# Kernel tuning notes

Hardware: AMD Instinct MI355X
Metric: run time of the kernel (lower is better)

Reference implementation:

```python
import jax, jax.numpy as jnp
import numpy as np

GAMMA = 20
LAMBDA_INV = 25.0


def setup_inputs() -> dict:
    key = jax.random.key(0)
    k1, k2 = jax.random.split(key)
    B, P, D = 128, 512, 384
    z = jax.random.normal(k1, (B, P, D), dtype=jnp.float32)
    view_ids = jax.random.randint(k2, (P,), 0, 2, dtype=jnp.int64)
    return {"z": z, "view_ids": view_ids}


def reference(z, view_ids):
    B, P, D = z.shape
    # [B, P, P] pairwise similarity per image
    sim = jnp.einsum('bpd,bqd->bpq', z, z)
    # valid pairs: different view and not self
    mask_view = view_ids[None, :] != view_ids[:, None]          # [P, P]
    mask = mask_view & ~jnp.eye(P, dtype=bool)
    sim = jnp.where(mask[None, :, :], sim, jnp.float32(-1.0))
    best_sim = sim.max(axis=2)                                   # [B, P]
    best_j = sim.argmax(axis=2)                                  # [B, P]
    # flatten across batch, global top-gamma anchors
    best_sim_flat = best_sim.reshape(-1)                         # [B*P]
    offsets = jnp.arange(B, dtype=best_j.dtype)[:, None] * P
    best_j_flat = (best_j + offsets).reshape(-1)                 # [B*P]
    topk_vals, topk_idx = jax.lax.top_k(best_sim_flat, GAMMA)
    z_flat = z.reshape(-1, D)
    z1 = z_flat[topk_idx]                                        # anchors
    z2 = z_flat[best_j_flat[topk_idx]]                           # matches
    loss = LAMBDA_INV * jnp.mean((z1 - z2) ** 2)
    fmatch_avg_cos = jax.lax.stop_gradient(topk_vals.mean())
    return loss, fmatch_avg_cos
```

## Files before the change

kernel.cpp:

```cpp
#include <hip/hip_runtime.h>


#define NB 128
#define NP 512
#define ND 384
#define NGAMMA 20
#define NKS 12

typedef __attribute__((ext_vector_type(8))) short short8;
typedef __attribute__((ext_vector_type(4))) float f32x4;

__device__ __forceinline__ unsigned short f2bf(float f) {
    unsigned int u = __float_as_uint(f);
    u += 0x7fffu + ((u >> 16) & 1u);
    return (unsigned short)(u >> 16);
}

__device__ __forceinline__ void gload16(const void* gptr, void* lptr) {
    __builtin_amdgcn_global_load_lds(
        (const __attribute__((address_space(1))) void*)gptr,
        (__attribute__((address_space(3))) void*)lptr, 16, 0, 0);
}

__global__ __launch_bounds__(256) void fm_convert(
    const float* __restrict__ z, unsigned short* __restrict__ zhi)
{
    size_t i = (size_t)blockIdx.x * 256 + threadIdx.x;
    const float4* zp = (const float4*)z + i * 2;
    float4 v0 = zp[0], v1 = zp[1];
    float f[8] = {v0.x, v0.y, v0.z, v0.w, v1.x, v1.y, v1.z, v1.w};
    short8 s;
#pragma unroll
    for (int j = 0; j < 8; ++j) s[j] = (short)f2bf(f[j]);
    *(short8*)&zhi[i * 8] = s;
}

__global__ __launch_bounds__(256, 3) void fm_gemm(
    const unsigned short* __restrict__ zhi, const int* __restrict__ view,
    float* __restrict__ pval, int* __restrict__ pidx)
{
    __shared__ __align__(16) unsigned short Ah[3][4][128][8];
    __shared__ __align__(16) unsigned short Bh[3][4][128][8];
    __shared__ int vs[NP];
    float* lsv = (float*)&Ah[0][0][0][0];
    int*   lsi = (int*)lsv + 256;
    float* lqv = (float*)((int*)lsv + 512);
    int*   lqi = (int*)lsv + 768;

    const int tid  = threadIdx.x;
    const int lane = tid & 63;
    const int wid  = tid >> 6;
    const int wr   = wid >> 1, wc = wid & 1;
    const int g    = lane >> 4, r = lane & 15;

    const int bid  = blockIdx.x;
    const int gidx = (bid & 7) * 160 + (bid >> 3);
    const int b    = gidx / 10;
    const int t    = gidx % 10;
    int tr, tc;
    if (t < 4)      { tr = 0; tc = t; }
    else if (t < 7) { tr = 1; tc = t - 3; }
    else if (t < 9) { tr = 2; tc = t - 5; }
    else            { tr = 3; tc = 3; }
    const bool diag = (tr == tc);
    const int p0 = tr * 128, q0 = tc * 128;

    vs[tid]       = view[tid];
    vs[tid + 256] = view[tid + 256];
    __builtin_amdgcn_sched_barrier(0);

    const size_t zb = (size_t)b * NP * ND;

    f32x4 acc[4][4];
#pragma unroll
    for (int mi = 0; mi < 4; ++mi)
#pragma unroll
        for (int ni = 0; ni < 4; ++ni) acc[mi][ni] = (f32x4){0.f, 0.f, 0.f, 0.f};

#define STAGE(BUF, KT)                                                           \
    do {                                                                         \
        _Pragma("unroll")                                                        \
        for (int i = 0; i < 2; ++i) {                                            \
            const int c_  = wid * 2 + i;                                         \
            const int kg_ = c_ >> 1;                                             \
            const int rb_ = (c_ & 1) * 64;                                       \
            gload16(zhi + zb + (size_t)(p0 + rb_ + lane) * ND + (KT) * 32 + kg_ * 8, \
                    &Ah[BUF][kg_][rb_][0]);                                      \
            gload16(zhi + zb + (size_t)(q0 + rb_ + lane) * ND + (KT) * 32 + kg_ * 8, \
                    &Bh[BUF][kg_][rb_][0]);                                      \
        }                                                                        \
    } while (0)

#define COMPUTE(BUF)                                                             \
    do {                                                                         \
        short8 ah_[4], bh_[4];                                                   \
        _Pragma("unroll")                                                        \
        for (int mi = 0; mi < 4; ++mi)                                           \
            ah_[mi] = *(const short8*)&Ah[BUF][g][wr * 64 + mi * 16 + r][0];     \
        _Pragma("unroll")                                                        \
        for (int ni = 0; ni < 4; ++ni)                                           \
            bh_[ni] = *(const short8*)&Bh[BUF][g][wc * 64 + ni * 16 + r][0];     \
        _Pragma("unroll")                                                        \
        for (int mi = 0; mi < 4; ++mi)                                           \
            _Pragma("unroll")                                                    \
            for (int ni = 0; ni < 4; ++ni)                                       \
                acc[mi][ni] = __builtin_amdgcn_mfma_f32_16x16x32_bf16(           \
                    ah_[mi], bh_[ni], acc[mi][ni], 0, 0, 0);                     \
    } while (0)

    STAGE(0, 0);
    STAGE(1, 1);
#pragma unroll
    for (int kt = 0; kt < NKS; ++kt) {
        if (kt < NKS - 1) asm volatile("s_waitcnt vmcnt(4)" ::: "memory");
        else              asm volatile("s_waitcnt vmcnt(0)" ::: "memory");
        __builtin_amdgcn_s_barrier();
        __builtin_amdgcn_sched_barrier(0);
        if (kt + 2 < NKS) STAGE((kt + 2) % 3, kt + 2);
        __builtin_amdgcn_sched_barrier(0);
        COMPUTE(kt % 3);
    }
#undef STAGE
#undef COMPUTE

#pragma unroll
    for (int mi = 0; mi < 4; ++mi) {
#pragma unroll
        for (int j = 0; j < 4; ++j) {
            const int prow = p0 + wr * 64 + mi * 16 + g * 4 + j;
            const int rv = vs[prow];
            float bv = -2.0f; int bq = 0;
#pragma unroll
            for (int ni = 0; ni < 4; ++ni) {
                const int q = q0 + wc * 64 + ni * 16 + r;
                const float v = (vs[q] != rv) ? acc[mi][ni][j] : -1.0f;
                if (v > bv) { bv = v; bq = q; }
            }
#pragma unroll
            for (int off = 1; off < 16; off <<= 1) {
                const float ov = __shfl_xor(bv, off);
                const int   oq = __shfl_xor(bq, off);
                if (ov > bv || (ov == bv && oq < bq)) { bv = ov; bq = oq; }
            }
            if (r == 0) {
                lsv[(wr * 2 + wc) * 64 + mi * 16 + g * 4 + j] = bv;
                lsi[(wr * 2 + wc) * 64 + mi * 16 + g * 4 + j] = bq;
            }
        }
    }
    if (!diag) {
#pragma unroll
        for (int ni = 0; ni < 4; ++ni) {
            const int q = q0 + wc * 64 + ni * 16 + r;
            const int qv = vs[q];
            float bv = -2.0f; int bp = 0;
#pragma unroll
            for (int mi = 0; mi < 4; ++mi)
#pragma unroll
                for (int j = 0; j < 4; ++j) {
                    const int prow = p0 + wr * 64 + mi * 16 + g * 4 + j;
                    const float v = (vs[prow] != qv) ? acc[mi][ni][j] : -1.0f;
                    if (v > bv) { bv = v; bp = prow; }
                }
#pragma unroll
            for (int off = 16; off < 64; off <<= 1) {
                const float ov = __shfl_xor(bv, off);
                const int   op = __shfl_xor(bp, off);
                if (ov > bv || (ov == bv && op < bp)) { bv = ov; bp = op; }
            }
            if (g == 0) {
                lqv[(wc * 2 + wr) * 64 + ni * 16 + r] = bv;
                lqi[(wc * 2 + wr) * 64 + ni * 16 + r] = bp;
            }
        }
    }
    __syncthreads();
    if (tid < 128) {
        const int half = tid >> 6, row = tid & 63;
        {
            float v0 = lsv[(half * 2 + 0) * 64 + row]; int i0 = lsi[(half * 2 + 0) * 64 + row];
            const float v1 = lsv[(half * 2 + 1) * 64 + row]; const int i1 = lsi[(half * 2 + 1) * 64 + row];
            if (v1 > v0) { v0 = v1; i0 = i1; }
            const int p = p0 + half * 64 + row;
            pval[((size_t)b * NP + p) * 4 + tc] = v0;
            pidx[((size_t)b * NP + p) * 4 + tc] = i0;
        }
        if (!diag) {
            float v0 = lqv[(half * 2 + 0) * 64 + row]; int i0 = lqi[(half * 2 + 0) * 64 + row];
            const float v1 = lqv[(half * 2 + 1) * 64 + row]; const int i1 = lqi[(half * 2 + 1) * 64 + row];
            if (v1 > v0) { v0 = v1; i0 = i1; }
            const int q = q0 + half * 64 + row;
            pval[((size_t)b * NP + q) * 4 + tr] = v0;
            pidx[((size_t)b * NP + q) * 4 + tr] = i0;
        }
    }
}

__global__ __launch_bounds__(64) void fm_topk_local(
    const float* __restrict__ pval, float* __restrict__ cval, int* __restrict__ cidx)
{
    const int lane = threadIdx.x;
    const int base = blockIdx.x * 1024;
    float v[16]; int id[16];
#pragma unroll
    for (int i = 0; i < 16; ++i) {
        const int a = base + i * 64 + lane;
        const float4 pv = ((const float4*)pval)[a];
        float bv = pv.x;
        if (pv.y > bv) bv = pv.y;
        if (pv.z > bv) bv = pv.z;
        if (pv.w > bv) bv = pv.w;
        v[i] = bv; id[i] = a;
    }
    for (int it = 0; it < NGAMMA; ++it) {
        float bv = v[0]; int bi = id[0];
#pragma unroll
        for (int i = 1; i < 16; ++i)
            if (v[i] > bv || (v[i] == bv && id[i] < bi)) { bv = v[i]; bi = id[i]; }
#pragma unroll
        for (int off = 1; off < 64; off <<= 1) {
            const float ov = __shfl_xor(bv, off);
            const int   oi = __shfl_xor(bi, off);
            if (ov > bv || (ov == bv && oi < bi)) { bv = ov; bi = oi; }
        }
        if (lane == 0) {
            cval[blockIdx.x * NGAMMA + it] = bv;
            cidx[blockIdx.x * NGAMMA + it] = bi;
        }
#pragma unroll
        for (int i = 0; i < 16; ++i) if (id[i] == bi) v[i] = -1e30f;
    }
}

__global__ __launch_bounds__(256) void fm_final(
    const float* __restrict__ cval, const int* __restrict__ cidx,
    const float* __restrict__ pval, const int* __restrict__ pidx,
    const float* __restrict__ z, float* __restrict__ out)
{
    __shared__ int sel[NGAMMA];
    __shared__ int selj[NGAMMA];
    __shared__ float red[4];

    const int t = threadIdx.x;
    const int lane = t & 63, w = t >> 6;
    float ssum = 0.f;

    if (w == 0) {
        float v[20]; int id[20];
#pragma unroll
        for (int i = 0; i < 20; ++i) {
            const int e = i * 64 + lane;
            v[i] = cval[e]; id[i] = cidx[e];
        }
        for (int it = 0; it < NGAMMA; ++it) {
            float bv = v[0]; int bi = id[0];
#pragma unroll
            for (int i = 1; i < 20; ++i)
                if (v[i] > bv || (v[i] == bv && id[i] < bi)) { bv = v[i]; bi = id[i]; }
#pragma unroll
            for (int off = 1; off < 64; off <<= 1) {
                const float ov = __shfl_xor(bv, off);
                const int   oi = __shfl_xor(bi, off);
                if (ov > bv || (ov == bv && oi < bi)) { bv = ov; bi = oi; }
            }
            if (lane == 0) sel[it] = bi;
            ssum += bv;
#pragma unroll
            for (int i = 0; i < 20; ++i) if (id[i] == bi) v[i] = -1e30f;
        }
        if (lane < NGAMMA) {
            const int a = sel[lane];
            const float4 pv = ((const float4*)pval)[a];
            float bv = pv.x; int bc = 0;
            if (pv.y > bv) { bv = pv.y; bc = 1; }
            if (pv.z > bv) { bv = pv.z; bc = 2; }
            if (pv.w > bv) { bv = pv.w; bc = 3; }
            selj[lane] = ((a >> 9) << 9) + pidx[(size_t)a * 4 + bc];
        }
    }
    __syncthreads();

    float acc = 0.f;
    for (int pr = 0; pr < NGAMMA; ++pr) {
        const int a = sel[pr];
        const int j = selj[pr];
        const float* za = z + (size_t)a * ND;
        const float* zj = z + (size_t)j * ND;
        for (int d = t; d < ND; d += 256) {
            const float df = za[d] - zj[d];
            acc = fmaf(df, df, acc);
        }
    }
#pragma unroll
    for (int off = 1; off < 64; off <<= 1) acc += __shfl_xor(acc, off);
    if (lane == 0) red[w] = acc;
    __syncthreads();
    if (t == 0) {
        const float tot = red[0] + red[1] + red[2] + red[3];
        out[0] = 25.0f * tot / (float)(NGAMMA * ND);
        out[1] = ssum / (float)NGAMMA;
    }
}

extern "C" void kernel_launch(void* const* d_in, const int* in_sizes, int n_in,
                              void* d_out, int out_size, void* d_ws, size_t ws_size,
                              hipStream_t stream)
{
    const float* z    = (const float*)d_in[0];
    const int*   view = (const int*)d_in[1];
    float*       out  = (float*)d_out;
    char* ws = (char*)d_ws;

    const size_t zhi_off  = 0;
    const size_t pval_off = (size_t)NB * NP * ND * 2;
    const size_t pidx_off = pval_off + (size_t)NB * NP * 4 * 4;
    const size_t cval_off = pidx_off + (size_t)NB * NP * 4 * 4;
    const size_t cidx_off = cval_off + 64 * NGAMMA * 4;

    unsigned short* zhi = (unsigned short*)(ws + zhi_off);
    float* pval = (float*)(ws + pval_off);
    int*   pidx = (int*)(ws + pidx_off);
    float* cval = (float*)(ws + cval_off);
    int*   cidx = (int*)(ws + cidx_off);

    fm_convert<<<(NB * NP * ND) / (8 * 256), 256, 0, stream>>>(z, zhi);
    fm_gemm<<<NB * 10, 256, 0, stream>>>(zhi, view, pval, pidx);
    fm_topk_local<<<(NB * NP) / 1024, 64, 0, stream>>>(pval, cval, cidx);
    fm_final<<<1, 256, 0, stream>>>(cval, cidx, pval, pidx, z, out);
}
```

Baseline: 147.4 us.

## Store bf16 copy of z in k-tiled layout for contiguous GEMM staging loads

The conversion kernel now stages a 128x32 fp32 tile through shared memory and writes the bf16 output in a blocked layout grouped by batch, k-tile, 8-element k-group and row. The GEMM staging loads then read 64 consecutive 16-byte chunks per wave instead of strided 16-byte pieces from rows 768 bytes apart. The aim is coalesced global-to-LDS transfers in the GEMM, at the cost of an extra shared-memory pass and a barrier in the conversion kernel.

```diff
diff --git a/kernel.cpp b/kernel.cpp
--- a/kernel.cpp
+++ b/kernel.cpp
@@ -23,20 +23,46 @@
 }
 
 __global__ __launch_bounds__(256) void fm_convert(
-    const float* __restrict__ z, unsigned short* __restrict__ zhi)
-{
-    size_t i = (size_t)blockIdx.x * 256 + threadIdx.x;
-    const float4* zp = (const float4*)z + i * 2;
-    float4 v0 = zp[0], v1 = zp[1];
-    float f[8] = {v0.x, v0.y, v0.z, v0.w, v1.x, v1.y, v1.z, v1.w};
-    short8 s;
-#pragma unroll
-    for (int j = 0; j < 8; ++j) s[j] = (short)f2bf(f[j]);
-    *(short8*)&zhi[i * 8] = s;
+    const float* __restrict__ z, unsigned short* __restrict__ zt)
+{
+    __shared__ float ls[128][36];
+
+    const int tid  = threadIdx.x;
+    const int bid  = blockIdx.x;
+    const int b    = bid / (NKS * 4);
+    const int rem  = bid % (NKS * 4);
+    const int kt   = rem >> 2;
+    const int pblk = rem & 3;
+
+    const float* zsrc = z + ((size_t)b * NP + pblk * 128) * ND + kt * 32;
+#pragma unroll
+    for (int i = 0; i < 4; ++i) {
+        const int f   = tid + i * 256;
+        const int row = f >> 3, c4 = f & 7;
+        const float4 v = *(const float4*)(zsrc + (size_t)row * ND + c4 * 4);
+        *(float4*)&ls[row][c4 * 4] = v;
+    }
+    __syncthreads();
+
+    const int kg = tid >> 6, lane = tid & 63;
+    unsigned short* dst = zt + (((size_t)b * NKS + kt) * 4 + kg) * 4096
+                             + (size_t)pblk * 128 * 8;
+#pragma unroll
+    for (int it = 0; it < 2; ++it) {
+        const int row = it * 64 + lane;
+        const float4 v0 = *(const float4*)&ls[row][kg * 8];
+        const float4 v1 = *(const float4*)&ls[row][kg * 8 + 4];
+        short8 s;
+        s[0] = (short)f2bf(v0.x); s[1] = (short)f2bf(v0.y);
+        s[2] = (short)f2bf(v0.z); s[3] = (short)f2bf(v0.w);
+        s[4] = (short)f2bf(v1.x); s[5] = (short)f2bf(v1.y);
+        s[6] = (short)f2bf(v1.z); s[7] = (short)f2bf(v1.w);
+        *(short8*)(dst + (size_t)row * 8) = s;
+    }
 }
 
 __global__ __launch_bounds__(256, 3) void fm_gemm(
-    const unsigned short* __restrict__ zhi, const int* __restrict__ view,
+    const unsigned short* __restrict__ zt, const int* __restrict__ view,
     float* __restrict__ pval, int* __restrict__ pidx)
 {
     __shared__ __align__(16) unsigned short Ah[3][4][128][8];
@@ -69,8 +95,6 @@
     vs[tid + 256] = view[tid + 256];
     __builtin_amdgcn_sched_barrier(0);
 
-    const size_t zb = (size_t)b * NP * ND;
-
     f32x4 acc[4][4];
 #pragma unroll
     for (int mi = 0; mi < 4; ++mi)
@@ -84,9 +108,10 @@
             const int c_  = wid * 2 + i;                                         \
             const int kg_ = c_ >> 1;                                             \
             const int rb_ = (c_ & 1) * 64;                                       \
-            gload16(zhi + zb + (size_t)(p0 + rb_ + lane) * ND + (KT) * 32 + kg_ * 8, \
+            const size_t pl_ = (((size_t)b * NKS + (KT)) * 4 + kg_) * 4096;      \
+            gload16(zt + pl_ + (size_t)(p0 + rb_ + lane) * 8,                    \
                     &Ah[BUF][kg_][rb_][0]);                                      \
-            gload16(zhi + zb + (size_t)(q0 + rb_ + lane) * ND + (KT) * 32 + kg_ * 8, \
+            gload16(zt + pl_ + (size_t)(q0 + rb_ + lane) * 8,                    \
                     &Bh[BUF][kg_][rb_][0]);                                      \
         }                                                                        \
     } while (0)
@@ -311,20 +336,20 @@
     float*       out  = (float*)d_out;
     char* ws = (char*)d_ws;
 
-    const size_t zhi_off  = 0;
+    const size_t zt_off   = 0;
     const size_t pval_off = (size_t)NB * NP * ND * 2;
     const size_t pidx_off = pval_off + (size_t)NB * NP * 4 * 4;
     const size_t cval_off = pidx_off + (size_t)NB * NP * 4 * 4;
     const size_t cidx_off = cval_off + 64 * NGAMMA * 4;
 
-    unsigned short* zhi = (unsigned short*)(ws + zhi_off);
+    unsigned short* zt = (unsigned short*)(ws + zt_off);
     float* pval = (float*)(ws + pval_off);
     int*   pidx = (int*)(ws + pidx_off);
     float* cval = (float*)(ws + cval_off);
     int*   cidx = (int*)(ws + cidx_off);
 
-    fm_convert<<<(NB * NP * ND) / (8 * 256), 256, 0, stream>>>(z, zhi);
-    fm_gemm<<<NB * 10, 256, 0, stream>>>(zhi, view, pval, pidx);
+    fm_convert<<<NB * NKS * 4, 256, 0, stream>>>(z, zt);
+    fm_gemm<<<NB * 10, 256, 0, stream>>>(zt, view, pval, pidx);
     fm_topk_local<<<(NB * NP) / 1024, 64, 0, stream>>>(pval, cval, cidx);
     fm_final<<<1, 256, 0, stream>>>(cval, cidx, pval, pidx, z, out);
 }
```

Result: faster. 134.5 us (-8.7%).
